# Performance work log

Measured on AMD Instinct MI355X. Metric: run time of the kernel, lower is better.

The kernel has to match this reference:

```python
import jax, jax.numpy as jnp
import numpy as np

B, D, K, A = 32768, 256, 1024, 32
MIN_LOG_STD, MAX_LOG_STD = -20.0, 2.0


def setup_inputs() -> dict:
    key = jax.random.key(0)
    ks = jax.random.split(key, 9)
    return {
        "obs": jax.random.normal(ks[0], (B, D), dtype=jnp.float32),
        "mean_C": jax.random.normal(ks[1], (K, D), dtype=jnp.float32),
        "mean_sigma": jnp.abs(jax.random.normal(ks[2], (K,), dtype=jnp.float32)) + 0.1,
        "mean_w": jax.random.normal(ks[3], (A, K), dtype=jnp.float32),
        "mean_b": jax.random.normal(ks[4], (A,), dtype=jnp.float32),
        "std_C": jax.random.normal(ks[5], (K, D), dtype=jnp.float32),
        "std_sigma": jnp.abs(jax.random.normal(ks[6], (K,), dtype=jnp.float32)) + 0.1,
        "std_w": jax.random.normal(ks[7], (A, K), dtype=jnp.float32),
        "std_b": jax.random.normal(ks[8], (A,), dtype=jnp.float32),
    }


def _rbf(x, C, sigma_sq, w, b):
    # r[b,k] = sum_d (x[b,d] - C[k,d])^2, expanded to avoid a [B,K,D] intermediate
    x2 = jnp.sum(x * x, axis=-1, keepdims=True)           # [B,1]
    c2 = jnp.sum(C * C, axis=-1)[None, :]                  # [1,K]
    r = x2 - 2.0 * (x @ C.T) + c2                          # [B,K]
    phi = jnp.exp(-r / (2.0 * jnp.abs(sigma_sq)[None, :]))  # [B,K]
    return phi @ w.T + b[None, :]                          # [B,A]


def reference(obs, mean_C, mean_sigma, mean_w, mean_b,
              std_C, std_sigma, std_w, std_b):
    action_mean = _rbf(obs, mean_C, mean_sigma, mean_w, mean_b)
    std_raw = _rbf(obs, std_C, std_sigma, std_w, std_b)
    action_std = jnp.exp(jnp.clip(std_raw, MIN_LOG_STD, MAX_LOG_STD))
    return jnp.concatenate((action_mean, action_std), axis=-1)  # [B, 2A]
```

## Files before the change

### kernel.cpp

```cpp
#include <hip/hip_runtime.h>


typedef float floatx4 __attribute__((ext_vector_type(4)));
typedef unsigned short u16;
typedef unsigned int u32;
typedef unsigned char u8;

constexpr float LOG2E = 1.4426950408889634f;

__device__ __forceinline__ u32 pk_fp8(float a, float b, float c, float d) {
  u32 v = __builtin_amdgcn_cvt_pk_fp8_f32(a, b, 0u, 0);
  v = __builtin_amdgcn_cvt_pk_fp8_f32(c, d, v, 1);
  return v;
}
__device__ __forceinline__ long mk64(u32 lo, u32 hi) {
  return (long)lo | ((long)hi << 32);
}

__global__ void prep(const float* __restrict__ mC, const float* __restrict__ mS,
                     const float* __restrict__ sC, const float* __restrict__ sS,
                     const float* __restrict__ mw, const float* __restrict__ sw,
                     u8* __restrict__ Cb, float* __restrict__ c2g,
                     float* __restrict__ s2g, u8* __restrict__ wb)
{
  const int blk = blockIdx.x;
  if (blk < 512) {
    const int wv = threadIdx.x >> 6;
    const int l  = threadIdx.x & 63;
    const int b  = blk * 4 + wv;
    const int half = b >> 10;
    const int k = b & 1023;
    const float* src = (half ? sC : mC) + (size_t)k * 256;
    float4 f = *(const float4*)(src + l * 4);
    float ss = f.x*f.x + f.y*f.y + f.z*f.z + f.w*f.w;
    ((u32*)Cb)[b * 64 + l] = pk_fp8(f.x, f.y, f.z, f.w);
    for (int off = 32; off > 0; off >>= 1) ss += __shfl_down(ss, off, 64);
    if (l == 0) {
      c2g[b] = ss;
      float sig = (half ? sS : mS)[k];
      s2g[b] = LOG2E * 0.5f / fabsf(sig);
    }
  } else {
    int i0 = (blk - 512) * 1024 + threadIdx.x * 4;
    int half = i0 >> 15;
    int rem  = i0 & 32767;
    const float* src = half ? sw : mw;
    float4 f = *(const float4*)(src + rem);
    ((u32*)wb)[i0 >> 2] = pk_fp8(f.x, f.y, f.z, f.w);
  }
}

__device__ __forceinline__ void stage_tile(const u8* __restrict__ gtile,
                                           u8* __restrict__ ldst, int t)
{
  #pragma unroll
  for (int i = 0; i < 4; ++i) {
    int s   = i * 256 + t;
    int row = s >> 4;
    int l16 = (s & 15) ^ (row & 15);
    __builtin_amdgcn_global_load_lds(
        (const __attribute__((address_space(1))) u32*)(const void*)(gtile + row * 256 + l16 * 16),
        (__attribute__((address_space(3))) u32*)(void*)(ldst + s * 16),
        16, 0, 0);
  }
}

__device__ __forceinline__ long ld_frag8(const u8* __restrict__ lds, int row, int cc8) {
  int s16 = (cc8 >> 1) ^ (row & 15);
  return *(const long*)(lds + row * 256 + s16 * 16 + (cc8 & 1) * 8);
}

__global__ __launch_bounds__(256, 2)
void policy_main(const float* __restrict__ obs,
                 const u8* __restrict__ Cb,
                 const float* __restrict__ c2g,
                 const float* __restrict__ s2g,
                 const u8* __restrict__ wb,
                 const float* __restrict__ mbias,
                 const float* __restrict__ sbias,
                 float* __restrict__ out)
{
  __shared__ __align__(16) char smem[69632];
  u8* cs0 = (u8*)smem;
  u8* cs1 = (u8*)(smem + 16384);
  float* x2p = (float*)(smem + 32768);
  float* red = (float*)smem;

  const int tid  = threadIdx.x;
  const int lane = tid & 63;
  const int wv   = tid >> 6;
  const int c    = lane & 15;
  const int q    = lane >> 4;
  const int row0 = blockIdx.x * 64;

  stage_tile(Cb, cs0, tid);

  {
    #pragma unroll
    for (int i = 0; i < 4; ++i) {
      int s   = i * 256 + tid;
      int row = s >> 4;
      int s16 = s & 15;
      int l16 = s16 ^ (row & 15);
      const float* src = obs + (size_t)(row0 + row) * 256 + l16 * 16;
      float4 f0 = ((const float4*)src)[0];
      float4 f1 = ((const float4*)src)[1];
      float4 f2 = ((const float4*)src)[2];
      float4 f3 = ((const float4*)src)[3];
      uint4 pk;
      pk.x = pk_fp8(f0.x, f0.y, f0.z, f0.w);
      pk.y = pk_fp8(f1.x, f1.y, f1.z, f1.w);
      pk.z = pk_fp8(f2.x, f2.y, f2.z, f2.w);
      pk.w = pk_fp8(f3.x, f3.y, f3.z, f3.w);
      *(uint4*)(cs1 + s * 16) = pk;
      float p = f0.x*f0.x + f0.y*f0.y + f0.z*f0.z + f0.w*f0.w
              + f1.x*f1.x + f1.y*f1.y + f1.z*f1.z + f1.w*f1.w
              + f2.x*f2.x + f2.y*f2.y + f2.z*f2.z + f2.w*f2.w
              + f3.x*f3.x + f3.y*f3.y + f3.z*f3.z + f3.w*f3.w;
      x2p[row * 16 + s16] = p;
    }
  }
  __syncthreads();

  long ob[4][8];
  #pragma unroll
  for (int nt = 0; nt < 4; ++nt) {
    const int row = nt * 16 + c;
    #pragma unroll
    for (int ks = 0; ks < 8; ++ks)
      ob[nt][ks] = ld_frag8(cs1, row, 4 * ks + q);
  }
  if (tid < 64) {
    float4 a0 = ((const float4*)(x2p + tid * 16))[0];
    float4 a1 = ((const float4*)(x2p + tid * 16))[1];
    float4 a2v = ((const float4*)(x2p + tid * 16))[2];
    float4 a3 = ((const float4*)(x2p + tid * 16))[3];
    x2p[1024 + tid] = a0.x+a0.y+a0.z+a0.w + a1.x+a1.y+a1.z+a1.w
                    + a2v.x+a2v.y+a2v.z+a2v.w + a3.x+a3.y+a3.z+a3.w;
  }
  __syncthreads();

  float x2v[4];
  #pragma unroll
  for (int nt = 0; nt < 4; ++nt) x2v[nt] = x2p[1024 + nt * 16 + c];
  __syncthreads();

  floatx4 acc2m[2][4], acc2s[2][4];
  #pragma unroll
  for (int a2i = 0; a2i < 2; ++a2i)
    #pragma unroll
    for (int nt = 0; nt < 4; ++nt) {
      acc2m[a2i][nt] = (floatx4){0.f, 0.f, 0.f, 0.f};
      acc2s[a2i][nt] = (floatx4){0.f, 0.f, 0.f, 0.f};
    }

  u32 pE[4];
  const int crow = 16 * wv + c;
  const int kslc = 16 * wv + 4 * q;

  for (int ct = 0; ct < 32; ++ct) {
    const int p = ct & 1;
    u8* cur = p ? cs1 : cs0;
    u8* nxt = p ? cs0 : cs1;

    if (ct < 31) stage_tile(Cb + (size_t)(ct + 1) * 16384, nxt, tid);

    float4 c2a = *(const float4*)(c2g + ct * 64 + kslc);
    float4 s2a = *(const float4*)(s2g + ct * 64 + kslc);

    floatx4 acc1[4];
    #pragma unroll
    for (int nt = 0; nt < 4; ++nt) acc1[nt] = (floatx4){0.f, 0.f, 0.f, 0.f};
    #pragma unroll
    for (int ks = 0; ks < 8; ++ks) {
      long cf = ld_frag8(cur, crow, 4 * ks + q);
      acc1[0] = __builtin_amdgcn_mfma_f32_16x16x32_fp8_fp8(cf, ob[0][ks], acc1[0], 0, 0, 0);
      acc1[1] = __builtin_amdgcn_mfma_f32_16x16x32_fp8_fp8(cf, ob[1][ks], acc1[1], 0, 0, 0);
      acc1[2] = __builtin_amdgcn_mfma_f32_16x16x32_fp8_fp8(cf, ob[2][ks], acc1[2], 0, 0, 0);
      acc1[3] = __builtin_amdgcn_mfma_f32_16x16x32_fp8_fp8(cf, ob[3][ks], acc1[3], 0, 0, 0);
    }

    u32 pc[4];
    #pragma unroll
    for (int nt = 0; nt < 4; ++nt) {
      float p0 = __builtin_amdgcn_exp2f((2.f * acc1[nt][0] - x2v[nt] - c2a.x) * s2a.x);
      float p1 = __builtin_amdgcn_exp2f((2.f * acc1[nt][1] - x2v[nt] - c2a.y) * s2a.y);
      float p2 = __builtin_amdgcn_exp2f((2.f * acc1[nt][2] - x2v[nt] - c2a.z) * s2a.z);
      float p3 = __builtin_amdgcn_exp2f((2.f * acc1[nt][3] - x2v[nt] - c2a.w) * s2a.w);
      pc[nt] = pk_fp8(p0, p1, p2, p3);
    }

    if (!p) {
      #pragma unroll
      for (int nt = 0; nt < 4; ++nt) pE[nt] = pc[nt];
    } else {
      const int kbE = ((ct - 1) & 15) * 64 + kslc;
      if (ct < 16) {
        #pragma unroll
        for (int a2i = 0; a2i < 2; ++a2i) {
          const u8* wrow = wb + (size_t)(a2i * 16 + c) * 1024 + kbE;
          long a2 = mk64(*(const u32*)wrow, *(const u32*)(wrow + 64));
          #pragma unroll
          for (int nt = 0; nt < 4; ++nt)
            acc2m[a2i][nt] = __builtin_amdgcn_mfma_f32_16x16x32_fp8_fp8(
                a2, mk64(pE[nt], pc[nt]), acc2m[a2i][nt], 0, 0, 0);
        }
      } else {
        #pragma unroll
        for (int a2i = 0; a2i < 2; ++a2i) {
          const u8* wrow = wb + (size_t)(32 + a2i * 16 + c) * 1024 + kbE;
          long a2 = mk64(*(const u32*)wrow, *(const u32*)(wrow + 64));
          #pragma unroll
          for (int nt = 0; nt < 4; ++nt)
            acc2s[a2i][nt] = __builtin_amdgcn_mfma_f32_16x16x32_fp8_fp8(
                a2, mk64(pE[nt], pc[nt]), acc2s[a2i][nt], 0, 0, 0);
        }
      }
    }

    __syncthreads();
  }

  {
    float* myr = red + wv * 4352;
    #pragma unroll
    for (int a2i = 0; a2i < 2; ++a2i)
      #pragma unroll
      for (int nt = 0; nt < 4; ++nt) {
        *(floatx4*)(myr + (nt * 16 + c) * 68 + a2i * 16 + 4 * q)      = acc2m[a2i][nt];
        *(floatx4*)(myr + (nt * 16 + c) * 68 + 32 + a2i * 16 + 4 * q) = acc2s[a2i][nt];
      }
  }
  __syncthreads();

  #pragma unroll
  for (int i = 0; i < 16; ++i) {
    int idx = tid + 256 * i;
    int a = idx & 63;
    int b = idx >> 6;
    float v = red[b * 68 + a] + red[4352 + b * 68 + a] +
              red[8704 + b * 68 + a] + red[13056 + b * 68 + a];
    if (a < 32) {
      v += mbias[a];
    } else {
      v += sbias[a - 32];
      v = fminf(fmaxf(v, -20.f), 2.f);
      v = __builtin_amdgcn_exp2f(v * LOG2E);
    }
    out[(size_t)(row0 + b) * 64 + a] = v;
  }
}

extern "C" void kernel_launch(void* const* d_in, const int* in_sizes, int n_in,
                              void* d_out, int out_size, void* d_ws, size_t ws_size,
                              hipStream_t stream) {
  const float* obs = (const float*)d_in[0];
  const float* mC  = (const float*)d_in[1];
  const float* mS  = (const float*)d_in[2];
  const float* mW  = (const float*)d_in[3];
  const float* mB  = (const float*)d_in[4];
  const float* sC  = (const float*)d_in[5];
  const float* sS  = (const float*)d_in[6];
  const float* sW  = (const float*)d_in[7];
  const float* sB  = (const float*)d_in[8];
  float* out = (float*)d_out;

  u8*    Cb  = (u8*)d_ws;
  float* c2g = (float*)((char*)d_ws + 2048 * 256);
  float* s2g = c2g + 2048;
  u8*    wb  = (u8*)(s2g + 2048);

  prep<<<576, 256, 0, stream>>>(mC, mS, sC, sS, mW, sW, Cb, c2g, s2g, wb);
  policy_main<<<512, 256, 0, stream>>>(obs, Cb, c2g, s2g, wb, mB, sB, out);
}
```

Measured before the change: 137.6 us.

## Process centre tiles in pairs with quad-buffered LDS and folded exp constants

The main loop now handles two 64-centre tiles per iteration. Four LDS tile buffers are prefetched a full pair ahead, so there is one barrier per pair instead of one per tile, and the odd/even branch that buffered the first half of each second-stage operand goes away. The prep kernel now precomputes 2*s2 and -s2*c2, so each RBF exponent becomes one subtract plus one fma. The second-layer weight loads are issued at the top of each pair. In exchange the kernel uses more shared memory and more registers per thread, which could affect occupancy at two blocks per CU.

```diff
diff --git a/kernel.cpp b/kernel.cpp
--- a/kernel.cpp
+++ b/kernel.cpp
@@ -2,7 +2,6 @@
 
 
 typedef float floatx4 __attribute__((ext_vector_type(4)));
-typedef unsigned short u16;
 typedef unsigned int u32;
 typedef unsigned char u8;
 
@@ -20,8 +19,8 @@
 __global__ void prep(const float* __restrict__ mC, const float* __restrict__ mS,
                      const float* __restrict__ sC, const float* __restrict__ sS,
                      const float* __restrict__ mw, const float* __restrict__ sw,
-                     u8* __restrict__ Cb, float* __restrict__ c2g,
-                     float* __restrict__ s2g, u8* __restrict__ wb)
+                     u8* __restrict__ Cb, float* __restrict__ a2g,
+                     float* __restrict__ g2n, u8* __restrict__ wb)
 {
   const int blk = blockIdx.x;
   if (blk < 512) {
@@ -36,9 +35,10 @@
     ((u32*)Cb)[b * 64 + l] = pk_fp8(f.x, f.y, f.z, f.w);
     for (int off = 32; off > 0; off >>= 1) ss += __shfl_down(ss, off, 64);
     if (l == 0) {
-      c2g[b] = ss;
-      float sig = (half ? sS : mS)[k];
-      s2g[b] = LOG2E * 0.5f / fabsf(sig);
+      float sig = fabsf((half ? sS : mS)[k]);
+      float s2 = LOG2E * 0.5f / sig;
+      a2g[b] = 2.f * s2;
+      g2n[b] = -s2 * ss;
     }
   } else {
     int i0 = (blk - 512) * 1024 + threadIdx.x * 4;
@@ -50,40 +50,18 @@
   }
 }
 
-__device__ __forceinline__ void stage_tile(const u8* __restrict__ gtile,
-                                           u8* __restrict__ ldst, int t)
-{
-  #pragma unroll
-  for (int i = 0; i < 4; ++i) {
-    int s   = i * 256 + t;
-    int row = s >> 4;
-    int l16 = (s & 15) ^ (row & 15);
-    __builtin_amdgcn_global_load_lds(
-        (const __attribute__((address_space(1))) u32*)(const void*)(gtile + row * 256 + l16 * 16),
-        (__attribute__((address_space(3))) u32*)(void*)(ldst + s * 16),
-        16, 0, 0);
-  }
-}
-
-__device__ __forceinline__ long ld_frag8(const u8* __restrict__ lds, int row, int cc8) {
-  int s16 = (cc8 >> 1) ^ (row & 15);
-  return *(const long*)(lds + row * 256 + s16 * 16 + (cc8 & 1) * 8);
-}
-
 __global__ __launch_bounds__(256, 2)
 void policy_main(const float* __restrict__ obs,
                  const u8* __restrict__ Cb,
-                 const float* __restrict__ c2g,
-                 const float* __restrict__ s2g,
+                 const float* __restrict__ a2g,
+                 const float* __restrict__ g2n,
                  const u8* __restrict__ wb,
                  const float* __restrict__ mbias,
                  const float* __restrict__ sbias,
                  float* __restrict__ out)
 {
-  __shared__ __align__(16) char smem[69632];
-  u8* cs0 = (u8*)smem;
-  u8* cs1 = (u8*)(smem + 16384);
-  float* x2p = (float*)(smem + 32768);
+  __shared__ __align__(16) char smem[69888];
+  float* x2p = (float*)(smem + 65536);
   float* red = (float*)smem;
 
   const int tid  = threadIdx.x;
@@ -92,33 +70,51 @@
   const int c    = lane & 15;
   const int q    = lane >> 4;
   const int row0 = blockIdx.x * 64;
-
-  stage_tile(Cb, cs0, tid);
-
-  {
-    #pragma unroll
-    for (int i = 0; i < 4; ++i) {
-      int s   = i * 256 + tid;
-      int row = s >> 4;
-      int s16 = s & 15;
-      int l16 = s16 ^ (row & 15);
-      const float* src = obs + (size_t)(row0 + row) * 256 + l16 * 16;
-      float4 f0 = ((const float4*)src)[0];
-      float4 f1 = ((const float4*)src)[1];
-      float4 f2 = ((const float4*)src)[2];
-      float4 f3 = ((const float4*)src)[3];
-      uint4 pk;
-      pk.x = pk_fp8(f0.x, f0.y, f0.z, f0.w);
-      pk.y = pk_fp8(f1.x, f1.y, f1.z, f1.w);
-      pk.z = pk_fp8(f2.x, f2.y, f2.z, f2.w);
-      pk.w = pk_fp8(f3.x, f3.y, f3.z, f3.w);
-      *(uint4*)(cs1 + s * 16) = pk;
-      float p = f0.x*f0.x + f0.y*f0.y + f0.z*f0.z + f0.w*f0.w
-              + f1.x*f1.x + f1.y*f1.y + f1.z*f1.z + f1.w*f1.w
-              + f2.x*f2.x + f2.y*f2.y + f2.z*f2.z + f2.w*f2.w
-              + f3.x*f3.x + f3.y*f3.y + f3.z*f3.z + f3.w*f3.w;
-      x2p[row * 16 + s16] = p;
-    }
+  const int crow = 16 * wv + c;
+  const int kslc = 16 * wv + 4 * q;
+  const int ldl  = tid * 16;
+
+  int goff[4];
+  #pragma unroll
+  for (int i = 0; i < 4; ++i) {
+    int s = i * 256 + tid;
+    int row = s >> 4;
+    int l16 = (s & 15) ^ (row & 15);
+    goff[i] = row * 256 + l16 * 16;
+  }
+
+  #pragma unroll
+  for (int i = 0; i < 4; ++i) {
+    __builtin_amdgcn_global_load_lds(
+        (const __attribute__((address_space(1))) u32*)(const void*)(Cb + goff[i]),
+        (__attribute__((address_space(3))) u32*)(void*)(smem + i * 4096 + ldl), 16, 0, 0);
+    __builtin_amdgcn_global_load_lds(
+        (const __attribute__((address_space(1))) u32*)(const void*)(Cb + 16384 + goff[i]),
+        (__attribute__((address_space(3))) u32*)(void*)(smem + 16384 + i * 4096 + ldl), 16, 0, 0);
+  }
+
+  #pragma unroll
+  for (int i = 0; i < 4; ++i) {
+    int s = i * 256 + tid;
+    int row = s >> 4;
+    int s16 = s & 15;
+    int l16 = s16 ^ (row & 15);
+    const float* src = obs + (size_t)(row0 + row) * 256 + l16 * 16;
+    float4 f0 = ((const float4*)src)[0];
+    float4 f1 = ((const float4*)src)[1];
+    float4 f2 = ((const float4*)src)[2];
+    float4 f3 = ((const float4*)src)[3];
+    uint4 pk;
+    pk.x = pk_fp8(f0.x, f0.y, f0.z, f0.w);
+    pk.y = pk_fp8(f1.x, f1.y, f1.z, f1.w);
+    pk.z = pk_fp8(f2.x, f2.y, f2.z, f2.w);
+    pk.w = pk_fp8(f3.x, f3.y, f3.z, f3.w);
+    *(uint4*)(smem + 49152 + s * 16) = pk;
+    float p = f0.x*f0.x + f0.y*f0.y + f0.z*f0.z + f0.w*f0.w
+            + f1.x*f1.x + f1.y*f1.y + f1.z*f1.z + f1.w*f1.w
+            + f2.x*f2.x + f2.y*f2.y + f2.z*f2.z + f2.w*f2.w
+            + f3.x*f3.x + f3.y*f3.y + f3.z*f3.z + f3.w*f3.w;
+    x2p[row * 16 + s16] = p;
   }
   __syncthreads();
 
@@ -127,99 +123,129 @@
   for (int nt = 0; nt < 4; ++nt) {
     const int row = nt * 16 + c;
     #pragma unroll
-    for (int ks = 0; ks < 8; ++ks)
-      ob[nt][ks] = ld_frag8(cs1, row, 4 * ks + q);
+    for (int ks = 0; ks < 8; ++ks) {
+      int cc8 = 4 * ks + q;
+      int s16 = (cc8 >> 1) ^ (row & 15);
+      ob[nt][ks] = *(const long*)(smem + 49152 + row * 256 + s16 * 16 + (q & 1) * 8);
+    }
   }
   if (tid < 64) {
-    float4 a0 = ((const float4*)(x2p + tid * 16))[0];
-    float4 a1 = ((const float4*)(x2p + tid * 16))[1];
-    float4 a2v = ((const float4*)(x2p + tid * 16))[2];
-    float4 a3 = ((const float4*)(x2p + tid * 16))[3];
-    x2p[1024 + tid] = a0.x+a0.y+a0.z+a0.w + a1.x+a1.y+a1.z+a1.w
-                    + a2v.x+a2v.y+a2v.z+a2v.w + a3.x+a3.y+a3.z+a3.w;
+    float s = 0.f;
+    #pragma unroll
+    for (int j = 0; j < 16; j += 4) {
+      float4 a = *(const float4*)(x2p + tid * 16 + j);
+      s += a.x + a.y + a.z + a.w;
+    }
+    x2p[1024 + tid] = s;
   }
   __syncthreads();
 
-  float x2v[4];
-  #pragma unroll
-  for (int nt = 0; nt < 4; ++nt) x2v[nt] = x2p[1024 + nt * 16 + c];
-  __syncthreads();
-
+  float hx2[4];
+  #pragma unroll
+  for (int nt = 0; nt < 4; ++nt) hx2[nt] = 0.5f * x2p[1024 + nt * 16 + c];
+
+  int voff[8];
+  #pragma unroll
+  for (int ks = 0; ks < 8; ++ks) {
+    int cc8 = 4 * ks + q;
+    int s16 = (cc8 >> 1) ^ (crow & 15);
+    voff[ks] = crow * 256 + s16 * 16 + (q & 1) * 8;
+  }
+
+  const floatx4 Z4 = {0.f, 0.f, 0.f, 0.f};
   floatx4 acc2m[2][4], acc2s[2][4];
   #pragma unroll
   for (int a2i = 0; a2i < 2; ++a2i)
     #pragma unroll
     for (int nt = 0; nt < 4; ++nt) {
-      acc2m[a2i][nt] = (floatx4){0.f, 0.f, 0.f, 0.f};
-      acc2s[a2i][nt] = (floatx4){0.f, 0.f, 0.f, 0.f};
-    }
-
-  u32 pE[4];
-  const int crow = 16 * wv + c;
-  const int kslc = 16 * wv + 4 * q;
-
-  for (int ct = 0; ct < 32; ++ct) {
-    const int p = ct & 1;
-    u8* cur = p ? cs1 : cs0;
-    u8* nxt = p ? cs0 : cs1;
-
-    if (ct < 31) stage_tile(Cb + (size_t)(ct + 1) * 16384, nxt, tid);
-
-    float4 c2a = *(const float4*)(c2g + ct * 64 + kslc);
-    float4 s2a = *(const float4*)(s2g + ct * 64 + kslc);
-
-    floatx4 acc1[4];
-    #pragma unroll
-    for (int nt = 0; nt < 4; ++nt) acc1[nt] = (floatx4){0.f, 0.f, 0.f, 0.f};
-    #pragma unroll
-    for (int ks = 0; ks < 8; ++ks) {
-      long cf = ld_frag8(cur, crow, 4 * ks + q);
-      acc1[0] = __builtin_amdgcn_mfma_f32_16x16x32_fp8_fp8(cf, ob[0][ks], acc1[0], 0, 0, 0);
-      acc1[1] = __builtin_amdgcn_mfma_f32_16x16x32_fp8_fp8(cf, ob[1][ks], acc1[1], 0, 0, 0);
-      acc1[2] = __builtin_amdgcn_mfma_f32_16x16x32_fp8_fp8(cf, ob[2][ks], acc1[2], 0, 0, 0);
-      acc1[3] = __builtin_amdgcn_mfma_f32_16x16x32_fp8_fp8(cf, ob[3][ks], acc1[3], 0, 0, 0);
-    }
-
-    u32 pc[4];
-    #pragma unroll
-    for (int nt = 0; nt < 4; ++nt) {
-      float p0 = __builtin_amdgcn_exp2f((2.f * acc1[nt][0] - x2v[nt] - c2a.x) * s2a.x);
-      float p1 = __builtin_amdgcn_exp2f((2.f * acc1[nt][1] - x2v[nt] - c2a.y) * s2a.y);
-      float p2 = __builtin_amdgcn_exp2f((2.f * acc1[nt][2] - x2v[nt] - c2a.z) * s2a.z);
-      float p3 = __builtin_amdgcn_exp2f((2.f * acc1[nt][3] - x2v[nt] - c2a.w) * s2a.w);
-      pc[nt] = pk_fp8(p0, p1, p2, p3);
-    }
-
-    if (!p) {
-      #pragma unroll
-      for (int nt = 0; nt < 4; ++nt) pE[nt] = pc[nt];
-    } else {
-      const int kbE = ((ct - 1) & 15) * 64 + kslc;
-      if (ct < 16) {
-        #pragma unroll
-        for (int a2i = 0; a2i < 2; ++a2i) {
-          const u8* wrow = wb + (size_t)(a2i * 16 + c) * 1024 + kbE;
-          long a2 = mk64(*(const u32*)wrow, *(const u32*)(wrow + 64));
-          #pragma unroll
-          for (int nt = 0; nt < 4; ++nt)
-            acc2m[a2i][nt] = __builtin_amdgcn_mfma_f32_16x16x32_fp8_fp8(
-                a2, mk64(pE[nt], pc[nt]), acc2m[a2i][nt], 0, 0, 0);
-        }
-      } else {
-        #pragma unroll
-        for (int a2i = 0; a2i < 2; ++a2i) {
-          const u8* wrow = wb + (size_t)(32 + a2i * 16 + c) * 1024 + kbE;
-          long a2 = mk64(*(const u32*)wrow, *(const u32*)(wrow + 64));
-          #pragma unroll
-          for (int nt = 0; nt < 4; ++nt)
-            acc2s[a2i][nt] = __builtin_amdgcn_mfma_f32_16x16x32_fp8_fp8(
-                a2, mk64(pE[nt], pc[nt]), acc2s[a2i][nt], 0, 0, 0);
-        }
-      }
-    }
-
-    __syncthreads();
-  }
+      acc2m[a2i][nt] = Z4;
+      acc2s[a2i][nt] = Z4;
+    }
+
+  int cA = 0, cB = 16384, nA = 32768, nB = 49152;
+  u32 pE[4], pc[4];
+
+#define PAIR_BODY(ACC, HB)                                                              \
+  {                                                                                     \
+    const int cte = 2 * pr;                                                             \
+    if (pr < 15) {                                                                      \
+      const u8* g0 = Cb + (size_t)(cte + 2) * 16384;                                    \
+      _Pragma("unroll")                                                                 \
+      for (int i = 0; i < 4; ++i) {                                                     \
+        __builtin_amdgcn_global_load_lds(                                               \
+            (const __attribute__((address_space(1))) u32*)(const void*)(g0 + goff[i]),  \
+            (__attribute__((address_space(3))) u32*)(void*)(smem + nA + i * 4096 + ldl),\
+            16, 0, 0);                                                                  \
+        __builtin_amdgcn_global_load_lds(                                               \
+            (const __attribute__((address_space(1))) u32*)(const void*)(g0 + 16384 + goff[i]), \
+            (__attribute__((address_space(3))) u32*)(void*)(smem + nB + i * 4096 + ldl),\
+            16, 0, 0);                                                                  \
+      }                                                                                 \
+    }                                                                                   \
+    float4 a2e = *(const float4*)(a2g + cte * 64 + kslc);                               \
+    float4 g2e = *(const float4*)(g2n + cte * 64 + kslc);                               \
+    float4 a2o = *(const float4*)(a2g + cte * 64 + 64 + kslc);                          \
+    float4 g2o = *(const float4*)(g2n + cte * 64 + 64 + kslc);                          \
+    const int kbE = (cte & 15) * 64 + kslc;                                             \
+    const u8* wr0 = wb + (size_t)(HB + c) * 1024 + kbE;                                 \
+    const u8* wr1 = wb + (size_t)(HB + 16 + c) * 1024 + kbE;                            \
+    u32 w0lo = *(const u32*)wr0, w0hi = *(const u32*)(wr0 + 64);                        \
+    u32 w1lo = *(const u32*)wr1, w1hi = *(const u32*)(wr1 + 64);                        \
+    floatx4 a1[4];                                                                      \
+    { long cf = *(const long*)(smem + cA + voff[0]);                                    \
+      _Pragma("unroll")                                                                 \
+      for (int nt = 0; nt < 4; ++nt)                                                    \
+        a1[nt] = __builtin_amdgcn_mfma_f32_16x16x32_fp8_fp8(cf, ob[nt][0], Z4, 0, 0, 0); } \
+    _Pragma("unroll")                                                                   \
+    for (int ks = 1; ks < 8; ++ks) {                                                    \
+      long cf = *(const long*)(smem + cA + voff[ks]);                                   \
+      _Pragma("unroll")                                                                 \
+      for (int nt = 0; nt < 4; ++nt)                                                    \
+        a1[nt] = __builtin_amdgcn_mfma_f32_16x16x32_fp8_fp8(cf, ob[nt][ks], a1[nt], 0, 0, 0); \
+    }                                                                                   \
+    _Pragma("unroll")                                                                   \
+    for (int nt = 0; nt < 4; ++nt) {                                                    \
+      float t0 = a1[nt][0] - hx2[nt], t1 = a1[nt][1] - hx2[nt];                         \
+      float t2 = a1[nt][2] - hx2[nt], t3 = a1[nt][3] - hx2[nt];                         \
+      pE[nt] = pk_fp8(__builtin_amdgcn_exp2f(fmaf(a2e.x, t0, g2e.x)),                   \
+                      __builtin_amdgcn_exp2f(fmaf(a2e.y, t1, g2e.y)),                   \
+                      __builtin_amdgcn_exp2f(fmaf(a2e.z, t2, g2e.z)),                   \
+                      __builtin_amdgcn_exp2f(fmaf(a2e.w, t3, g2e.w)));                  \
+    }                                                                                   \
+    { long cf = *(const long*)(smem + cB + voff[0]);                                    \
+      _Pragma("unroll")                                                                 \
+      for (int nt = 0; nt < 4; ++nt)                                                    \
+        a1[nt] = __builtin_amdgcn_mfma_f32_16x16x32_fp8_fp8(cf, ob[nt][0], Z4, 0, 0, 0); } \
+    _Pragma("unroll")                                                                   \
+    for (int ks = 1; ks < 8; ++ks) {                                                    \
+      long cf = *(const long*)(smem + cB + voff[ks]);                                   \
+      _Pragma("unroll")                                                                 \
+      for (int nt = 0; nt < 4; ++nt)                                                    \
+        a1[nt] = __builtin_amdgcn_mfma_f32_16x16x32_fp8_fp8(cf, ob[nt][ks], a1[nt], 0, 0, 0); \
+    }                                                                                   \
+    _Pragma("unroll")                                                                   \
+    for (int nt = 0; nt < 4; ++nt) {                                                    \
+      float t0 = a1[nt][0] - hx2[nt], t1 = a1[nt][1] - hx2[nt];                         \
+      float t2 = a1[nt][2] - hx2[nt], t3 = a1[nt][3] - hx2[nt];                         \
+      pc[nt] = pk_fp8(__builtin_amdgcn_exp2f(fmaf(a2o.x, t0, g2o.x)),                   \
+                      __builtin_amdgcn_exp2f(fmaf(a2o.y, t1, g2o.y)),                   \
+                      __builtin_amdgcn_exp2f(fmaf(a2o.z, t2, g2o.z)),                   \
+                      __builtin_amdgcn_exp2f(fmaf(a2o.w, t3, g2o.w)));                  \
+    }                                                                                   \
+    { long wA0 = mk64(w0lo, w0hi), wA1 = mk64(w1lo, w1hi);                              \
+      _Pragma("unroll")                                                                 \
+      for (int nt = 0; nt < 4; ++nt) {                                                  \
+        long pb = mk64(pE[nt], pc[nt]);                                                 \
+        ACC[0][nt] = __builtin_amdgcn_mfma_f32_16x16x32_fp8_fp8(wA0, pb, ACC[0][nt], 0, 0, 0); \
+        ACC[1][nt] = __builtin_amdgcn_mfma_f32_16x16x32_fp8_fp8(wA1, pb, ACC[1][nt], 0, 0, 0); \
+      } }                                                                               \
+    __syncthreads();                                                                    \
+    { int t_ = cA; cA = nA; nA = t_; t_ = cB; cB = nB; nB = t_; }                       \
+  }
+
+  for (int pr = 0; pr < 8; ++pr) PAIR_BODY(acc2m, 0)
+  for (int pr = 8; pr < 16; ++pr) PAIR_BODY(acc2s, 32)
+#undef PAIR_BODY
 
   {
     float* myr = red + wv * 4352;
@@ -266,10 +292,10 @@
   float* out = (float*)d_out;
 
   u8*    Cb  = (u8*)d_ws;
-  float* c2g = (float*)((char*)d_ws + 2048 * 256);
-  float* s2g = c2g + 2048;
-  u8*    wb  = (u8*)(s2g + 2048);
-
-  prep<<<576, 256, 0, stream>>>(mC, mS, sC, sS, mW, sW, Cb, c2g, s2g, wb);
-  policy_main<<<512, 256, 0, stream>>>(obs, Cb, c2g, s2g, wb, mB, sB, out);
-}
+  float* a2g = (float*)((char*)d_ws + 2048 * 256);
+  float* g2n = a2g + 2048;
+  u8*    wb  = (u8*)(g2n + 2048);
+
+  prep<<<576, 256, 0, stream>>>(mC, mS, sC, sS, mW, sW, Cb, a2g, g2n, wb);
+  policy_main<<<512, 256, 0, stream>>>(obs, Cb, a2g, g2n, wb, mB, sB, out);
+}
```

Result: faster. 133.2 us (-3.2%).
